# Kernel tuning notes

Hardware: AMD Instinct MI355X
Metric: run time of the kernel (lower is better)

## Reference

```python
import jax, jax.numpy as jnp
import numpy as np

KERNEL_SIZE = 9
STRIDE = 1
LN_EPS = 1e-5


def _toeplitz(L, dtype):
    # T[t, l] = 1 iff l - t == STRIDE * i for i in range(KERNEL_SIZE // STRIDE)
    d = jnp.arange(L)[None, :] - jnp.arange(L)[:, None]
    mask = (d >= 0) & (d % STRIDE == 0) & ((d // STRIDE) < (KERNEL_SIZE // STRIDE))
    return mask.astype(dtype)


def setup_inputs() -> dict:
    key = jax.random.key(0)
    ks = jax.random.split(key, 4)
    N, Cin, L, V = 16, 256, 300, 25
    P, Cout = 3, 256
    x = jax.random.normal(ks[0], (N, Cin, L, V), dtype=jnp.float32)
    A = jax.random.uniform(ks[1], (P, V, V), dtype=jnp.float32)
    conv_w = jax.random.normal(ks[2], (Cout * P, Cin), dtype=jnp.float32) * 0.02
    conv_b = jax.random.normal(ks[3], (Cout * P,), dtype=jnp.float32) * 0.02
    ln_gamma = jnp.ones((Cout, 1, V), dtype=jnp.float32)
    ln_beta = jnp.zeros((Cout, 1, V), dtype=jnp.float32)
    edge_importance = jnp.ones((P, V * V), dtype=jnp.float32)
    return {"x": x, "A": A, "conv_w": conv_w, "conv_b": conv_b,
            "ln_gamma": ln_gamma, "ln_beta": ln_beta,
            "edge_importance": edge_importance}


def reference(x, A, conv_w, conv_b, ln_gamma, ln_beta, edge_importance):
    N, Cin, L, V = x.shape
    P = A.shape[0]
    Cout = conv_w.shape[0] // P

    res = x  # in_channels == out_channels and stride == 1 -> identity residual

    # 1x1 conv -> (N, Cout*P, L, V); split into P chunks of Cout along channels
    y = jnp.einsum('nclv,oc->nolv', x, conv_w) + conv_b[None, :, None, None]
    y = y.reshape(N, P, Cout, L, V)  # chunk p == channels [p*Cout:(p+1)*Cout]

    # partitioned graph aggregation with edge importance: (P,V,V) adjacency
    Aw = A * edge_importance.reshape(P, V, V)
    y = jnp.einsum('npclv,pvw->npclw', y, Aw)  # (N, P, Cout, L, V)

    # temporal conv via toeplitz matmul over frame dim L
    T = _toeplitz(L, y.dtype)
    y = jnp.einsum('npclv,lm->npcmv', y, T)  # (N, P, Cout, L, V)

    # sum over partitions -> (N, Cout, L, V)
    y = y.sum(axis=1)

    # LayerNorm over (C, V) per (n, l), affine params shaped (Cout, 1, V)
    mu = jnp.mean(y, axis=(1, 3), keepdims=True)
    var = jnp.var(y, axis=(1, 3), keepdims=True)
    y = (y - mu) * jax.lax.rsqrt(var + LN_EPS)
    y = y * ln_gamma[None] + ln_beta[None]
    y = jax.nn.relu(y)

    # residual add, final ReLU (dropout rate 0.0 -> identity)
    return jax.nn.relu(y + res)
```

## Files before the change

kernel.cpp:

```cpp
#include <hip/hip_runtime.h>

#define NN 16
#define CIN 256
#define COUT 256
#define LL 300
#define VV 25
#define PP 3
#define KS 9
#define KK 768
#define MM (NN*LL*VV)
#define MPAD 120064
#define MBLK 938

typedef float floatx4 __attribute__((ext_vector_type(4)));
typedef short short8 __attribute__((ext_vector_type(8)));

__device__ __forceinline__ unsigned short f2bf(float f) {
    unsigned u = __builtin_bit_cast(unsigned, f);
    u += 0x7fff + ((u >> 16) & 1);
    return (unsigned short)(u >> 16);
}
__device__ __forceinline__ float bf2f(unsigned short h) {
    unsigned u = ((unsigned)h) << 16;
    return __builtin_bit_cast(float, u);
}
__device__ __forceinline__ void gl2lds16(const void* g, void* l) {
    __builtin_amdgcn_global_load_lds(
        (const __attribute__((address_space(1))) void*)g,
        (__attribute__((address_space(3))) void*)l, 16, 0, 0);
}

__global__ __launch_bounds__(256) void k_prep(
    const float* __restrict__ A, const float* __restrict__ conv_w,
    const float* __restrict__ conv_b, const float* __restrict__ ei,
    unsigned short* __restrict__ w2t, float* __restrict__ bias2,
    unsigned short* __restrict__ xa)
{
    const int t = blockIdx.x * 256 + threadIdx.x;
    const int nthr = gridDim.x * 256;
    for (int idx = t; idx < COUT * KK; idx += nthr) {
        int c = idx / KK, k = idx % KK, p = k >> 8, ci = k & 255;
        w2t[idx] = f2bf(conv_w[(p * COUT + c) * CIN + ci]);
    }
    for (int idx = t; idx < COUT * VV; idx += nthr) {
        int c = idx / VV, w = idx % VV;
        float s = 0.f;
        for (int p = 0; p < PP; ++p) {
            float cs = 0.f;
            for (int v = 0; v < VV; ++v) {
                int a = (p * VV + v) * VV + w;
                cs += A[a] * ei[a];
            }
            s += conv_b[p * COUT + c] * cs;
        }
        bias2[idx] = s;
    }
    for (int idx = t; idx < (MPAD - MM) * KK; idx += nthr)
        xa[(size_t)MM * KK + idx] = 0;
}

__global__ __launch_bounds__(256) void k_agg(
    const float* __restrict__ x, const float* __restrict__ A,
    const float* __restrict__ ei, unsigned short* __restrict__ xa)
{
    __shared__ float Aw[PP * VV * VV];
    const int l = blockIdx.x, n = blockIdx.y, t = threadIdx.x;
    for (int idx = t; idx < PP * VV * VV; idx += 256)
        Aw[idx] = A[idx] * ei[idx];
    __syncthreads();

    float xv[VV];
    const float* xp = x + ((size_t)(n * CIN + t) * LL + l) * VV;
    #pragma unroll
    for (int v = 0; v < VV; ++v) xv[v] = xp[v];

    const size_t mrow = (size_t)(n * LL + l) * VV;
    #pragma unroll
    for (int p = 0; p < PP; ++p) {
        float acc[VV];
        #pragma unroll
        for (int w = 0; w < VV; ++w) acc[w] = 0.f;
        #pragma unroll
        for (int v = 0; v < VV; ++v) {
            const float xvv = xv[v];
            const float* ar = &Aw[(p * VV + v) * VV];
            #pragma unroll
            for (int w = 0; w < VV; ++w) acc[w] += xvv * ar[w];
        }
        #pragma unroll
        for (int w = 0; w < VV; ++w)
            xa[(mrow + w) * KK + p * CIN + t] = f2bf(acc[w]);
    }
}

__global__ __launch_bounds__(256) void k_gemm(
    const unsigned short* __restrict__ xa,
    const unsigned short* __restrict__ w2t,
    unsigned short* __restrict__ z)
{
    __shared__ __align__(16) unsigned short As[128 * 32];
    __shared__ __align__(16) unsigned short Bs[128 * 32];
    const int t = threadIdx.x, wv = t >> 6, ln = t & 63;
    const int m0 = blockIdx.x * 128, c0 = blockIdx.y * 128;

    floatx4 acc[4][4];
    #pragma unroll
    for (int i = 0; i < 4; ++i)
        #pragma unroll
        for (int j = 0; j < 4; ++j)
            acc[i][j] = (floatx4){0.f, 0.f, 0.f, 0.f};

    const int srow = wv * 32 + (ln >> 2);
    const int scol = (ln & 3) * 8;
    const int mw = (wv >> 1) * 64, nw = (wv & 1) * 64;
    const int frow = ln & 15, fcol = (ln >> 4) * 8;

    for (int kt = 0; kt < KK / 32; ++kt) {
        const int k0 = kt * 32;
        __syncthreads();
        gl2lds16(xa  + (size_t)(m0 + srow)      * KK + k0 + scol, &As[(wv * 32) * 32]);
        gl2lds16(xa  + (size_t)(m0 + srow + 16) * KK + k0 + scol, &As[(wv * 32 + 16) * 32]);
        gl2lds16(w2t + (size_t)(c0 + srow)      * KK + k0 + scol, &Bs[(wv * 32) * 32]);
        gl2lds16(w2t + (size_t)(c0 + srow + 16) * KK + k0 + scol, &Bs[(wv * 32 + 16) * 32]);
        __syncthreads();

        short8 af[4], bf[4];
        #pragma unroll
        for (int i = 0; i < 4; ++i)
            af[i] = *(const short8*)&As[(mw + i * 16 + frow) * 32 + fcol];
        #pragma unroll
        for (int j = 0; j < 4; ++j)
            bf[j] = *(const short8*)&Bs[(nw + j * 16 + frow) * 32 + fcol];
        #pragma unroll
        for (int i = 0; i < 4; ++i)
            #pragma unroll
            for (int j = 0; j < 4; ++j)
                acc[i][j] = __builtin_amdgcn_mfma_f32_16x16x32_bf16(af[j] * 0 + af[i], bf[j], acc[i][j], 0, 0, 0);
    }

    const int q = ln >> 4, cL = ln & 15;
    #pragma unroll
    for (int i = 0; i < 4; ++i) {
        #pragma unroll
        for (int j = 0; j < 4; ++j) {
            #pragma unroll
            for (int r = 0; r < 4; ++r) {
                const int m = m0 + mw + i * 16 + q * 4 + r;
                const int c = c0 + nw + j * 16 + cL;
                if (m < MM) z[(size_t)m * COUT + c] = f2bf(acc[i][j][r]);
            }
        }
    }
}

__global__ __launch_bounds__(256) void k_ln(
    const unsigned short* __restrict__ z, const float* __restrict__ x,
    const float* __restrict__ bias2, const float* __restrict__ gamma,
    const float* __restrict__ beta, float* __restrict__ out)
{
    const int m = blockIdx.x, n = blockIdx.y, t = threadIdx.x;
    float zw[VV];
    #pragma unroll
    for (int w = 0; w < VV; ++w) zw[w] = 0.f;

    const int l0 = (m >= KS - 1) ? (m - (KS - 1)) : 0;
    for (int l = l0; l <= m; ++l) {
        const unsigned short* zp = z + (size_t)((n * LL + l) * VV) * COUT + t;
        #pragma unroll
        for (int w = 0; w < VV; ++w) zw[w] += bf2f(zp[(size_t)w * COUT]);
    }
    const float cnt = (float)(m - l0 + 1);
    const float* b2 = bias2 + t * VV;
    #pragma unroll
    for (int w = 0; w < VV; ++w) zw[w] += cnt * b2[w];

    float s1 = 0.f, s2 = 0.f;
    #pragma unroll
    for (int w = 0; w < VV; ++w) { s1 += zw[w]; s2 += zw[w] * zw[w]; }

    __shared__ float rs[4], rq[4], stats[2];
    #pragma unroll
    for (int off = 32; off; off >>= 1) { s1 += __shfl_down(s1, off); s2 += __shfl_down(s2, off); }
    const int wid = t >> 6, lane = t & 63;
    if (lane == 0) { rs[wid] = s1; rq[wid] = s2; }
    __syncthreads();
    if (t == 0) {
        const float S1 = rs[0] + rs[1] + rs[2] + rs[3];
        const float S2 = rq[0] + rq[1] + rq[2] + rq[3];
        const float inv = 1.f / (COUT * VV);
        const float mu = S1 * inv;
        const float var = S2 * inv - mu * mu;
        stats[0] = mu;
        stats[1] = rsqrtf(var + 1e-5f);
    }
    __syncthreads();
    const float mu = stats[0], rsd = stats[1];

    const float* gp = gamma + t * VV;
    const float* bp = beta + t * VV;
    const float* xp = x + ((size_t)(n * CIN + t) * LL + m) * VV;
    float* op = out + ((size_t)(n * COUT + t) * LL + m) * VV;
    #pragma unroll
    for (int w = 0; w < VV; ++w) {
        float val = (zw[w] - mu) * rsd * gp[w] + bp[w];
        val = fmaxf(val, 0.f);
        val += xp[w];
        op[w] = fmaxf(val, 0.f);
    }
}

extern "C" void kernel_launch(void* const* d_in, const int* in_sizes, int n_in,
                              void* d_out, int out_size, void* d_ws, size_t ws_size,
                              hipStream_t stream) {
    const float* x      = (const float*)d_in[0];
    const float* A      = (const float*)d_in[1];
    const float* conv_w = (const float*)d_in[2];
    const float* conv_b = (const float*)d_in[3];
    const float* gamma  = (const float*)d_in[4];
    const float* beta   = (const float*)d_in[5];
    const float* ei     = (const float*)d_in[6];
    float* out = (float*)d_out;

    char* ws = (char*)d_ws;
    unsigned short* xa  = (unsigned short*)ws;
    unsigned short* z   = (unsigned short*)(ws + 184418304);
    unsigned short* w2t = (unsigned short*)(ws + 245891072);
    float*          b2  = (float*)(ws + 246284288);

    k_prep<<<64, 256, 0, stream>>>(A, conv_w, conv_b, ei, w2t, b2, xa);
    k_agg<<<dim3(LL, NN), 256, 0, stream>>>(x, A, ei, xa);
    k_gemm<<<dim3(MBLK, 2), 256, 0, stream>>>(xa, w2t, z);
    k_ln<<<dim3(LL, NN), 256, 0, stream>>>(z, x, b2, gamma, beta, out);
}
```

Before: 592.4 us.

## Pad adjacency rows for vector LDS reads, drop dummy MFMA operand, XCD-aware LN grid

The aggregation kernel stores the weighted adjacency in shared memory with rows padded to 28 floats, so each thread reads it as float4 vectors instead of scalars. The GEMM inner loop drops a redundant `af[j]*0 + af[i]` expression that added vector multiply work before every MFMA. The LayerNorm kernel switches to a 1D grid with block indices remapped so each XCD handles a contiguous range of frames, which is meant to improve L2 reuse of the overlapping 9-frame windows of z. The remap launches a few extra blocks that exit immediately.

```diff
diff --git a/kernel.cpp b/kernel.cpp
--- a/kernel.cpp
+++ b/kernel.cpp
@@ -5,12 +5,15 @@
 #define COUT 256
 #define LL 300
 #define VV 25
+#define VP 28
 #define PP 3
 #define KS 9
 #define KK 768
 #define MM (NN*LL*VV)
 #define MPAD 120064
 #define MBLK 938
+#define XCDS 8
+#define MPX 38
 
 typedef float floatx4 __attribute__((ext_vector_type(4)));
 typedef short short8 __attribute__((ext_vector_type(8)));
@@ -63,10 +66,12 @@
     const float* __restrict__ x, const float* __restrict__ A,
     const float* __restrict__ ei, unsigned short* __restrict__ xa)
 {
-    __shared__ float Aw[PP * VV * VV];
+    __shared__ float AwL[PP * VV * VP];
     const int l = blockIdx.x, n = blockIdx.y, t = threadIdx.x;
-    for (int idx = t; idx < PP * VV * VV; idx += 256)
-        Aw[idx] = A[idx] * ei[idx];
+    for (int idx = t; idx < PP * VV * VV; idx += 256) {
+        int pv = idx / VV, w = idx % VV;
+        AwL[pv * VP + w] = A[idx] * ei[idx];
+    }
     __syncthreads();
 
     float xv[VV];
@@ -83,9 +88,14 @@
         #pragma unroll
         for (int v = 0; v < VV; ++v) {
             const float xvv = xv[v];
-            const float* ar = &Aw[(p * VV + v) * VV];
+            const float* ar = &AwL[(p * VV + v) * VP];
             #pragma unroll
-            for (int w = 0; w < VV; ++w) acc[w] += xvv * ar[w];
+            for (int wq = 0; wq < 24; wq += 4) {
+                const float4 f = *(const float4*)(ar + wq);
+                acc[wq + 0] += xvv * f.x; acc[wq + 1] += xvv * f.y;
+                acc[wq + 2] += xvv * f.z; acc[wq + 3] += xvv * f.w;
+            }
+            acc[24] += xvv * ar[24];
         }
         #pragma unroll
         for (int w = 0; w < VV; ++w)
@@ -135,7 +145,7 @@
         for (int i = 0; i < 4; ++i)
             #pragma unroll
             for (int j = 0; j < 4; ++j)
-                acc[i][j] = __builtin_amdgcn_mfma_f32_16x16x32_bf16(af[j] * 0 + af[i], bf[j], acc[i][j], 0, 0, 0);
+                acc[i][j] = __builtin_amdgcn_mfma_f32_16x16x32_bf16(af[i], bf[j], acc[i][j], 0, 0, 0);
     }
 
     const int q = ln >> 4, cL = ln & 15;
@@ -158,7 +168,15 @@
     const float* __restrict__ bias2, const float* __restrict__ gamma,
     const float* __restrict__ beta, float* __restrict__ out)
 {
-    const int m = blockIdx.x, n = blockIdx.y, t = threadIdx.x;
+    const int b = blockIdx.x;
+    const int g = b & (XCDS - 1);
+    const int r = b >> 3;
+    const int mi = r % MPX;
+    const int n = r / MPX;
+    const int m = g * MPX + mi;
+    if (m >= LL) return;
+    const int t = threadIdx.x;
+
     float zw[VV];
     #pragma unroll
     for (int w = 0; w < VV; ++w) zw[w] = 0.f;
@@ -230,5 +248,5 @@
     k_prep<<<64, 256, 0, stream>>>(A, conv_w, conv_b, ei, w2t, b2, xa);
     k_agg<<<dim3(LL, NN), 256, 0, stream>>>(x, A, ei, xa);
     k_gemm<<<dim3(MBLK, 2), 256, 0, stream>>>(xa, w2t, z);
-    k_ln<<<dim3(LL, NN), 256, 0, stream>>>(z, x, b2, gamma, beta, out);
-}
+    k_ln<<<XCDS * NN * MPX, 256, 0, stream>>>(z, x, b2, gamma, beta, out);
+}
```

Measured after the change: 550.5 us. 7.1% less time.
